# Kernel optimization log

Hardware: AMD Instinct MI355X
Metric: run time of the kernel (lower is better)

Reference implementation:

```python
import jax, jax.numpy as jnp
import numpy as np
from jax import lax

BN_EPS = 1e-5
DELTA_FRAC = 0.7


def ternarize(t):
    """Per-row (dim 0) ternarization: delta = 0.7*mean|t_i|, alpha = mean of |t_i| above delta."""
    B = t.shape[0]
    flat = t.reshape(B, -1)                       # [B, n]
    absf = jnp.abs(flat)
    n = flat.shape[1]
    d = DELTA_FRAC * absf.sum(axis=1) / n         # [B]
    mask = absf > d[:, None]                      # strict >, matching torch code
    count = mask.sum(axis=1).astype(flat.dtype)
    alpha = (absf * mask).sum(axis=1) / count     # [B]
    tern = jnp.where(flat > d[:, None], 1.0, 0.0) + jnp.where(flat < -d[:, None], -1.0, 0.0)
    return (tern * alpha[:, None]).reshape(t.shape)


def conv2d(x, w, b):
    out = lax.conv_general_dilated(x, w, window_strides=(1, 1), padding='VALID',
                                   dimension_numbers=('NCHW', 'OIHW', 'NCHW'))
    return out + b[None, :, None, None]


def maxpool2(x):
    return lax.reduce_window(x, -jnp.inf, lax.max, (1, 1, 2, 2), (1, 1, 2, 2), 'VALID')


def batchnorm_eval(x, gamma, beta):
    # eval-mode BN with running_mean=0, running_var=1
    inv = 1.0 / np.sqrt(1.0 + BN_EPS)
    return x * (gamma[None, :, None, None] * inv) + beta[None, :, None, None]


def setup_inputs() -> dict:
    key = jax.random.key(0)
    ks = jax.random.split(key, 12)
    B = 2048
    inp = {
        'x': jax.random.normal(ks[0], (B, 1, 28, 28), dtype=jnp.float32),
        'conv1_w': jax.random.normal(ks[1], (32, 1, 5, 5), dtype=jnp.float32) * 0.1,
        'conv1_b': jax.random.normal(ks[2], (32,), dtype=jnp.float32) * 0.1,
        'bn1_g': jax.random.normal(ks[3], (32,), dtype=jnp.float32) * 0.1 + 1.0,
        'bn1_b': jax.random.normal(ks[4], (32,), dtype=jnp.float32) * 0.1,
        'conv2_w': jax.random.normal(ks[5], (64, 32, 5, 5), dtype=jnp.float32) * 0.05,
        'conv2_b': jax.random.normal(ks[6], (64,), dtype=jnp.float32) * 0.1,
        'bn2_g': jax.random.normal(ks[7], (64,), dtype=jnp.float32) * 0.1 + 1.0,
        'bn2_b': jax.random.normal(ks[8], (64,), dtype=jnp.float32) * 0.1,
        'fc1_w': jax.random.normal(ks[9], (512, 1024), dtype=jnp.float32) * 0.03,
        'fc1_b': jax.random.normal(ks[10], (512,), dtype=jnp.float32) * 0.1,
        'fc2_w': jax.random.normal(ks[11], (10, 512), dtype=jnp.float32) * 0.05,
        'fc2_b': jnp.zeros((10,), dtype=jnp.float32),
    }
    return inp


def reference(x, conv1_w, conv1_b, bn1_g, bn1_b, conv2_w, conv2_b, bn2_g, bn2_b,
              fc1_w, fc1_b, fc2_w, fc2_b):
    h = ternarize(conv2d(x, conv1_w, conv1_b))            # [B,32,24,24]
    h = jax.nn.relu(maxpool2(batchnorm_eval(h, bn1_g, bn1_b)))  # [B,32,12,12]
    h = ternarize(conv2d(h, conv2_w, conv2_b))            # [B,64,8,8]
    h = jax.nn.relu(maxpool2(batchnorm_eval(h, bn2_g, bn2_b)))  # [B,64,4,4]
    h = h.reshape(-1, 1024)
    h = jax.nn.relu(ternarize(h @ fc1_w.T + fc1_b))       # [B,512]
    out = ternarize(h @ fc2_w.T + fc2_b)                  # [B,10]
    return out
```

## Files before the change

kernel.cpp:

```cpp
#include <hip/hip_runtime.h>

#define BATCH 2048

__device__ __forceinline__ float blockReduceSumF(float v, float* red, int tid, int nwaves) {
  #pragma unroll
  for (int off = 32; off > 0; off >>= 1) v += __shfl_xor(v, off);
  __syncthreads();
  if ((tid & 63) == 0) red[tid >> 6] = v;
  __syncthreads();
  if (tid == 0) {
    float s = red[0];
    for (int i = 1; i < nwaves; i++) s += red[i];
    red[31] = s;
  }
  __syncthreads();
  return red[31];
}

__device__ __forceinline__ float2 blockReduceSum2F(float a, float b, float* red, int tid, int nwaves) {
  #pragma unroll
  for (int off = 32; off > 0; off >>= 1) { a += __shfl_xor(a, off); b += __shfl_xor(b, off); }
  __syncthreads();
  if ((tid & 63) == 0) { red[tid >> 6] = a; red[(tid >> 6) + 16] = b; }
  __syncthreads();
  if (tid == 0) {
    float sa = red[0], sb = red[16];
    for (int i = 1; i < nwaves; i++) { sa += red[i]; sb += red[16 + i]; }
    red[30] = sa; red[31] = sb;
  }
  __syncthreads();
  return make_float2(red[30], red[31]);
}

__device__ __forceinline__ float groupReduce4w(float v, float* seg, int tj) {
  #pragma unroll
  for (int off = 32; off > 0; off >>= 1) v += __shfl_xor(v, off);
  __syncthreads();
  if ((tj & 63) == 0) seg[tj >> 6] = v;
  __syncthreads();
  return (seg[0] + seg[1]) + (seg[2] + seg[3]);
}

__global__ void k0_w2t(const float* __restrict__ w2, float* __restrict__ w2t) {
  int i = blockIdx.x * 256 + threadIdx.x;
  if (i >= 51200) return;
  int c2 = i / 800;
  int r = i - c2 * 800;
  w2t[r * 64 + c2] = w2[i];
}

__global__ __launch_bounds__(512, 6) void k1_conv1(
    const float* __restrict__ x, const float* __restrict__ w1, const float* __restrict__ b1,
    signed char* __restrict__ s1full, float* __restrict__ alpha1) {
  __shared__ float xs[784];
  __shared__ float wsm[800];
  __shared__ float red[32];

  const int tid = threadIdx.x;
  const int smp = blockIdx.x;

  for (int j = tid; j < 784; j += 512) xs[j] = x[smp * 784 + j];
  for (int j = tid; j < 800; j += 512) wsm[j] = w1[j];
  __syncthreads();

  const int c = tid >> 4;
  const int g = tid & 15;
  const float bias = b1[c];
  const float* wc = &wsm[c * 25];

  float a[36];
  float asum = 0.0f;
  #pragma unroll
  for (int tt = 0; tt < 3; tt++) {
    const int t = g + (tt << 4);
    const int r = t >> 1;
    const int hx = (t & 1) * 12;
    float acc[12];
    #pragma unroll
    for (int i = 0; i < 12; i++) acc[i] = bias;
    #pragma unroll
    for (int ky = 0; ky < 5; ky++) {
      const float* xp = &xs[(r + ky) * 28 + hx];
      float xrow[16];
      *(float4*)&xrow[0]  = *(const float4*)&xp[0];
      *(float4*)&xrow[4]  = *(const float4*)&xp[4];
      *(float4*)&xrow[8]  = *(const float4*)&xp[8];
      *(float4*)&xrow[12] = *(const float4*)&xp[12];
      #pragma unroll
      for (int kx = 0; kx < 5; kx++) {
        const float w = wc[ky * 5 + kx];
        #pragma unroll
        for (int i = 0; i < 12; i++) acc[i] = fmaf(xrow[i + kx], w, acc[i]);
      }
    }
    #pragma unroll
    for (int i = 0; i < 12; i++) { a[tt * 12 + i] = acc[i]; asum += fabsf(acc[i]); }
  }

  float tot = blockReduceSumF(asum, red, tid, 8);
  float delta = (0.7f * tot) / 18432.0f;

  float msum = 0.0f, mcnt = 0.0f;
  #pragma unroll
  for (int i = 0; i < 36; i++) {
    float fa = fabsf(a[i]);
    if (fa > delta) { msum += fa; mcnt += 1.0f; }
  }
  float2 mm = blockReduceSum2F(msum, mcnt, red, tid, 8);
  if (tid == 0) alpha1[smp] = (mm.y > 0.0f) ? (mm.x / mm.y) : 0.0f;

  signed char* sp = s1full + (size_t)smp * 18432 + c * 576 + g * 12;
  #pragma unroll
  for (int tt = 0; tt < 3; tt++) {
    #pragma unroll
    for (int i = 0; i < 12; i++) {
      float v = a[tt * 12 + i];
      int sv = (v > delta) ? 1 : ((v < -delta) ? -1 : 0);
      sp[tt * 192 + i] = (signed char)sv;
    }
  }
}

__global__ __launch_bounds__(256, 6) void k2_conv2(
    const signed char* __restrict__ s1full, const float* __restrict__ alpha1,
    const float* __restrict__ w2t, const float* __restrict__ b2,
    const float* __restrict__ g1, const float* __restrict__ bt1,
    signed char* __restrict__ s2full, float* __restrict__ alpha2) {
  __shared__ float pooled[4608];
  __shared__ float g1l[32], bt1l[32];
  __shared__ float red[32];

  const int tid = threadIdx.x;
  const int smp = blockIdx.x;
  const float BNINV = (float)(1.0 / sqrt(1.0 + 1e-5));

  if (tid < 32) { g1l[tid] = g1[tid] * BNINV; bt1l[tid] = bt1[tid]; }
  __syncthreads();

  const float a1 = alpha1[smp];
  for (int j = tid; j < 4608; j += 256) {
    int cc = j / 144;
    int r = j - cc * 144;
    int py = r / 12;
    int px = r - py * 12;
    const signed char* sp = s1full + (size_t)smp * 18432 + cc * 576 + (py * 2) * 24 + px * 2;
    float m = -1e30f;
    #pragma unroll
    for (int dy = 0; dy < 2; dy++)
      #pragma unroll
      for (int dx = 0; dx < 2; dx++) {
        float v = ((float)sp[dy * 24 + dx] * a1) * g1l[cc] + bt1l[cc];
        m = (v > m) ? v : m;
      }
    pooled[j] = (m > 0.0f) ? m : 0.0f;
  }
  __syncthreads();

  const int c2 = tid >> 2;
  const int q = tid & 3;
  const int r0 = q << 1;
  const float bias = b2[c2];
  float acc0[8], acc1[8];
  #pragma unroll
  for (int i = 0; i < 8; i++) { acc0[i] = bias; acc1[i] = bias; }

  for (int cc = 0; cc < 32; cc++) {
    const float* wt = w2t + cc * 1600 + c2;
    const float* pb = &pooled[cc * 144];
    float rows[2][12];
    *(float4*)&rows[0][0] = *(const float4*)&pb[r0 * 12];
    *(float4*)&rows[0][4] = *(const float4*)&pb[r0 * 12 + 4];
    *(float4*)&rows[0][8] = *(const float4*)&pb[r0 * 12 + 8];
    #pragma unroll
    for (int ky = 0; ky < 5; ky++) {
      float* B = rows[(ky + 1) & 1];
      const float* bp = &pb[(r0 + ky + 1) * 12];
      *(float4*)&B[0] = *(const float4*)&bp[0];
      *(float4*)&B[4] = *(const float4*)&bp[4];
      *(float4*)&B[8] = *(const float4*)&bp[8];
      const float* A = rows[ky & 1];
      #pragma unroll
      for (int kx = 0; kx < 5; kx++) {
        const float w = wt[(ky * 5 + kx) << 6];
        #pragma unroll
        for (int ox = 0; ox < 8; ox++) acc0[ox] = fmaf(A[ox + kx], w, acc0[ox]);
        #pragma unroll
        for (int ox = 0; ox < 8; ox++) acc1[ox] = fmaf(B[ox + kx], w, acc1[ox]);
      }
    }
  }

  float asum = 0.0f;
  #pragma unroll
  for (int i = 0; i < 8; i++) asum += fabsf(acc0[i]) + fabsf(acc1[i]);
  float tot = blockReduceSumF(asum, red, tid, 4);
  float delta = (0.7f * tot) / 4096.0f;

  float msum = 0.0f, mcnt = 0.0f;
  #pragma unroll
  for (int i = 0; i < 8; i++) {
    float f0 = fabsf(acc0[i]);
    if (f0 > delta) { msum += f0; mcnt += 1.0f; }
    float f1 = fabsf(acc1[i]);
    if (f1 > delta) { msum += f1; mcnt += 1.0f; }
  }
  float2 mm = blockReduceSum2F(msum, mcnt, red, tid, 4);
  if (tid == 0) alpha2[smp] = (mm.y > 0.0f) ? (mm.x / mm.y) : 0.0f;

  signed char* so = s2full + (size_t)smp * 4096 + c2 * 64 + r0 * 8;
  #pragma unroll
  for (int ox = 0; ox < 8; ox++) {
    float v = acc0[ox];
    so[ox] = (signed char)((v > delta) ? 1 : ((v < -delta) ? -1 : 0));
  }
  #pragma unroll
  for (int ox = 0; ox < 8; ox++) {
    float v = acc1[ox];
    so[8 + ox] = (signed char)((v > delta) ? 1 : ((v < -delta) ? -1 : 0));
  }
}

__global__ void k0_transpose(const float* __restrict__ w1f, float* __restrict__ w1t) {
  int i = blockIdx.x * 256 + threadIdx.x;
  int k = i >> 9;
  int o = i & 511;
  w1t[i] = w1f[o * 1024 + k];
}

__global__ __launch_bounds__(1024, 4) void k3_fc(
    const signed char* __restrict__ s2full, const float* __restrict__ alpha2,
    const float* __restrict__ w1t, const float* __restrict__ f1b,
    const float* __restrict__ w2f, const float* __restrict__ f2b,
    const float* __restrict__ g2, const float* __restrict__ bt2,
    float* __restrict__ out) {
  __shared__ float S[16384];
  __shared__ float fco[4][512];
  __shared__ float g2l[64], bt2l[64];
  __shared__ float redm[4][4];
  __shared__ float out2[4][10];

  const int tid = threadIdx.x;
  const int blk = blockIdx.x;
  const float BNINV = (float)(1.0 / sqrt(1.0 + 1e-5));

  if (tid < 64) { g2l[tid] = g2[tid] * BNINV; bt2l[tid] = bt2[tid]; }
  __syncthreads();

  float* h4 = S;
  for (int e = tid; e < 4096; e += 1024) {
    int j = e >> 2;
    int s = e & 3;
    int cc = j >> 4;
    int r = j & 15;
    int py = r >> 2;
    int px = r & 3;
    const signed char* sp = s2full + (size_t)(blk * 4 + s) * 4096 + cc * 64 + (py * 2) * 8 + px * 2;
    float a2 = alpha2[blk * 4 + s];
    float m = -1e30f;
    #pragma unroll
    for (int dy = 0; dy < 2; dy++)
      #pragma unroll
      for (int dx = 0; dx < 2; dx++) {
        float v = ((float)sp[dy * 8 + dx] * a2) * g2l[cc] + bt2l[cc];
        m = (v > m) ? v : m;
      }
    h4[j * 4 + s] = (m > 0.0f) ? m : 0.0f;
  }
  __syncthreads();

  const int kp = tid >> 7;
  const int og = tid & 127;
  float a00=0,a01=0,a02=0,a03=0, a10=0,a11=0,a12=0,a13=0;
  float a20=0,a21=0,a22=0,a23=0, a30=0,a31=0,a32=0,a33=0;
  const float4* w4 = (const float4*)w1t;
  const float4* h44 = (const float4*)h4;
  const int kbase = kp << 7;
  for (int kk = 0; kk < 128; kk++) {
    const int k = kbase + kk;
    const float4 wv = w4[(k << 7) + og];
    const float4 hv = h44[k];
    a00 = fmaf(hv.x, wv.x, a00); a01 = fmaf(hv.y, wv.x, a01);
    a02 = fmaf(hv.z, wv.x, a02); a03 = fmaf(hv.w, wv.x, a03);
    a10 = fmaf(hv.x, wv.y, a10); a11 = fmaf(hv.y, wv.y, a11);
    a12 = fmaf(hv.z, wv.y, a12); a13 = fmaf(hv.w, wv.y, a13);
    a20 = fmaf(hv.x, wv.z, a20); a21 = fmaf(hv.y, wv.z, a21);
    a22 = fmaf(hv.z, wv.z, a22); a23 = fmaf(hv.w, wv.z, a23);
    a30 = fmaf(hv.x, wv.w, a30); a31 = fmaf(hv.y, wv.w, a31);
    a32 = fmaf(hv.z, wv.w, a32); a33 = fmaf(hv.w, wv.w, a33);
  }
  __syncthreads();
  {
    float4* p4 = (float4*)S;
    const int base = (kp << 9) + (og << 2);
    p4[base + 0] = make_float4(a00, a01, a02, a03);
    p4[base + 1] = make_float4(a10, a11, a12, a13);
    p4[base + 2] = make_float4(a20, a21, a22, a23);
    p4[base + 3] = make_float4(a30, a31, a32, a33);
  }
  __syncthreads();

  for (int p = tid; p < 2048; p += 1024) {
    int o = p >> 2;
    int s = p & 3;
    float v = S[p];
    #pragma unroll
    for (int kp2 = 1; kp2 < 8; kp2++) v += S[kp2 * 2048 + p];
    fco[s][o] = v + f1b[o];
  }
  __syncthreads();

  float (*h3)[512] = (float(*)[512])S;
  const int sg = tid >> 8;
  const int tj = tid & 255;
  float v0 = fco[sg][tj];
  float v1 = fco[sg][tj + 256];
  float av0 = fabsf(v0), av1 = fabsf(v1);
  float tot = groupReduce4w(av0 + av1, redm[sg], tj);
  float delta = (0.7f * tot) / 512.0f;
  float m0 = (av0 > delta) ? av0 : 0.0f;
  float m1 = (av1 > delta) ? av1 : 0.0f;
  float msum = groupReduce4w(m0 + m1, redm[sg], tj);
  float mcnt = groupReduce4w(((av0 > delta) ? 1.0f : 0.0f) + ((av1 > delta) ? 1.0f : 0.0f),
                             redm[sg], tj);
  float alpha3 = (mcnt > 0.0f) ? (msum / mcnt) : 0.0f;
  {
    float t0 = (v0 > delta) ? 1.0f : ((v0 < -delta) ? -1.0f : 0.0f);
    float hv0 = t0 * alpha3;
    h3[sg][tj] = (hv0 > 0.0f) ? hv0 : 0.0f;
    float t1 = (v1 > delta) ? 1.0f : ((v1 < -delta) ? -1.0f : 0.0f);
    float hv1 = t1 * alpha3;
    h3[sg][tj + 256] = (hv1 > 0.0f) ? hv1 : 0.0f;
  }
  __syncthreads();

  const int lane = tid & 63;
  const int wid = tid >> 6;
  for (int t = wid; t < 40; t += 16) {
    int s = t / 10;
    int o = t - s * 10;
    float acc = 0.0f;
    #pragma unroll
    for (int m = 0; m < 8; m++) {
      int j = lane + (m << 6);
      acc = fmaf(h3[s][j], w2f[o * 512 + j], acc);
    }
    #pragma unroll
    for (int off = 32; off > 0; off >>= 1) acc += __shfl_xor(acc, off);
    if (lane == 0) out2[s][o] = acc + f2b[o];
  }
  __syncthreads();

  if (tid < 4) {
    int s = tid;
    float t2 = 0.0f;
    for (int i = 0; i < 10; i++) t2 += fabsf(out2[s][i]);
    float d = (0.7f * t2) / 10.0f;
    float ms = 0.0f, mc = 0.0f;
    for (int i = 0; i < 10; i++) {
      float a = fabsf(out2[s][i]);
      if (a > d) { ms += a; mc += 1.0f; }
    }
    float al = (mc > 0.0f) ? (ms / mc) : 0.0f;
    for (int i = 0; i < 10; i++) {
      float vv = out2[s][i];
      float sv = (vv > d) ? 1.0f : ((vv < -d) ? -1.0f : 0.0f);
      out[(size_t)(blk * 4 + s) * 10 + i] = sv * al;
    }
  }
}

__global__ void k_marker(float* __restrict__ out, int n, float val) {
  int i = blockIdx.x * 256 + threadIdx.x;
  if (i < n) out[i] = val;
}

extern "C" void kernel_launch(void* const* d_in, const int* in_sizes, int n_in,
                              void* d_out, int out_size, void* d_ws, size_t ws_size,
                              hipStream_t stream) {
  float* out = (float*)d_out;

  static const int expect[13] = {1605632, 800, 32, 32, 32, 51200, 64, 64, 64,
                                 524288, 512, 5120, 10};
  float marker = 0.0f;
  if (n_in != 13) marker = 304.0f;
  else {
    for (int i = 0; i < 13; i++)
      if (in_sizes[i] != expect[i]) { marker = 320.0f + 16.0f * i; break; }
  }
  if (marker == 0.0f && out_size != 20480) marker = 560.0f;

  float* alpha1 = (float*)d_ws;
  float* alpha2 = alpha1 + BATCH;
  float* w2t    = alpha2 + BATCH;
  signed char* s1full = (signed char*)(w2t + 51200);
  signed char* s2full = s1full + (size_t)BATCH * 18432;
  size_t needed = (size_t)((s2full + (size_t)BATCH * 4096) - (signed char*)d_ws);
  if (marker == 0.0f && ws_size < needed) marker = 576.0f;

  if (marker != 0.0f) {
    k_marker<<<dim3((out_size + 255) / 256), dim3(256), 0, stream>>>(out, out_size, marker);
    return;
  }

  const float* x   = (const float*)d_in[0];
  const float* c1w = (const float*)d_in[1];
  const float* c1b = (const float*)d_in[2];
  const float* g1  = (const float*)d_in[3];
  const float* bt1 = (const float*)d_in[4];
  const float* c2w = (const float*)d_in[5];
  const float* c2b = (const float*)d_in[6];
  const float* g2  = (const float*)d_in[7];
  const float* bt2 = (const float*)d_in[8];
  const float* f1w = (const float*)d_in[9];
  const float* f1b = (const float*)d_in[10];
  const float* f2w = (const float*)d_in[11];
  const float* f2b = (const float*)d_in[12];

  float* w1t = (float*)s1full;

  k0_w2t<<<dim3(200), dim3(256), 0, stream>>>(c2w, w2t);
  k1_conv1<<<dim3(BATCH), dim3(512), 0, stream>>>(x, c1w, c1b, s1full, alpha1);
  k2_conv2<<<dim3(BATCH), dim3(256), 0, stream>>>(s1full, alpha1, w2t, c2b, g1, bt1, s2full, alpha2);
  k0_transpose<<<dim3(2048), dim3(256), 0, stream>>>(f1w, w1t);
  k3_fc<<<dim3(BATCH / 4), dim3(1024), 0, stream>>>(s2full, alpha2, w1t, f1b, f2w, f2b, g2, bt2, out);
}
```

Baseline: 375.3 us.

## Process eight samples per FC block to halve fc1 weight traffic

```diff
diff --git a/kernel.cpp b/kernel.cpp
--- a/kernel.cpp
+++ b/kernel.cpp
@@ -32,13 +32,13 @@
   return make_float2(red[30], red[31]);
 }
 
-__device__ __forceinline__ float groupReduce4w(float v, float* seg, int tj) {
+__device__ __forceinline__ float groupReduce2w(float v, float* seg2, int tj) {
   #pragma unroll
   for (int off = 32; off > 0; off >>= 1) v += __shfl_xor(v, off);
   __syncthreads();
-  if ((tj & 63) == 0) seg[tj >> 6] = v;
-  __syncthreads();
-  return (seg[0] + seg[1]) + (seg[2] + seg[3]);
+  if ((tj & 63) == 0) seg2[tj >> 6] = v;
+  __syncthreads();
+  return seg2[0] + seg2[1];
 }
 
 __global__ void k0_w2t(const float* __restrict__ w2, float* __restrict__ w2t) {
@@ -227,35 +227,35 @@
   w1t[i] = w1f[o * 1024 + k];
 }
 
-__global__ __launch_bounds__(1024, 4) void k3_fc(
+__global__ __launch_bounds__(1024, 4) void k3_fc8(
     const signed char* __restrict__ s2full, const float* __restrict__ alpha2,
     const float* __restrict__ w1t, const float* __restrict__ f1b,
     const float* __restrict__ w2f, const float* __restrict__ f2b,
     const float* __restrict__ g2, const float* __restrict__ bt2,
     float* __restrict__ out) {
-  __shared__ float S[16384];
-  __shared__ float fco[4][512];
+  __shared__ float S[8192];
+  __shared__ float fco[8][512];
   __shared__ float g2l[64], bt2l[64];
-  __shared__ float redm[4][4];
-  __shared__ float out2[4][10];
+  __shared__ float seg[8][2];
+  __shared__ float out2[8][10];
 
   const int tid = threadIdx.x;
   const int blk = blockIdx.x;
   const float BNINV = (float)(1.0 / sqrt(1.0 + 1e-5));
 
   if (tid < 64) { g2l[tid] = g2[tid] * BNINV; bt2l[tid] = bt2[tid]; }
-  __syncthreads();
-
-  float* h4 = S;
-  for (int e = tid; e < 4096; e += 1024) {
-    int j = e >> 2;
-    int s = e & 3;
+  for (int p = tid; p < 4096; p += 1024) ((float*)fco)[p] = 0.0f;
+  __syncthreads();
+
+  for (int e = tid; e < 8192; e += 1024) {
+    int j = e >> 3;
+    int s = e & 7;
     int cc = j >> 4;
     int r = j & 15;
     int py = r >> 2;
     int px = r & 3;
-    const signed char* sp = s2full + (size_t)(blk * 4 + s) * 4096 + cc * 64 + (py * 2) * 8 + px * 2;
-    float a2 = alpha2[blk * 4 + s];
+    const signed char* sp = s2full + (size_t)(blk * 8 + s) * 4096 + cc * 64 + (py * 2) * 8 + px * 2;
+    float a2 = alpha2[blk * 8 + s];
     float m = -1e30f;
     #pragma unroll
     for (int dy = 0; dy < 2; dy++)
@@ -264,78 +264,83 @@
         float v = ((float)sp[dy * 8 + dx] * a2) * g2l[cc] + bt2l[cc];
         m = (v > m) ? v : m;
       }
-    h4[j * 4 + s] = (m > 0.0f) ? m : 0.0f;
+    S[j * 8 + s] = (m > 0.0f) ? m : 0.0f;
   }
   __syncthreads();
 
   const int kp = tid >> 7;
   const int og = tid & 127;
-  float a00=0,a01=0,a02=0,a03=0, a10=0,a11=0,a12=0,a13=0;
-  float a20=0,a21=0,a22=0,a23=0, a30=0,a31=0,a32=0,a33=0;
-  const float4* w4 = (const float4*)w1t;
-  const float4* h44 = (const float4*)h4;
-  const int kbase = kp << 7;
-  for (int kk = 0; kk < 128; kk++) {
-    const int k = kbase + kk;
-    const float4 wv = w4[(k << 7) + og];
-    const float4 hv = h44[k];
-    a00 = fmaf(hv.x, wv.x, a00); a01 = fmaf(hv.y, wv.x, a01);
-    a02 = fmaf(hv.z, wv.x, a02); a03 = fmaf(hv.w, wv.x, a03);
-    a10 = fmaf(hv.x, wv.y, a10); a11 = fmaf(hv.y, wv.y, a11);
-    a12 = fmaf(hv.z, wv.y, a12); a13 = fmaf(hv.w, wv.y, a13);
-    a20 = fmaf(hv.x, wv.z, a20); a21 = fmaf(hv.y, wv.z, a21);
-    a22 = fmaf(hv.z, wv.z, a22); a23 = fmaf(hv.w, wv.z, a23);
-    a30 = fmaf(hv.x, wv.w, a30); a31 = fmaf(hv.y, wv.w, a31);
-    a32 = fmaf(hv.z, wv.w, a32); a33 = fmaf(hv.w, wv.w, a33);
-  }
-  __syncthreads();
+  float ac[8][4];
+  #pragma unroll
+  for (int s = 0; s < 8; s++)
+    #pragma unroll
+    for (int i = 0; i < 4; i++) ac[s][i] = 0.0f;
+
   {
-    float4* p4 = (float4*)S;
-    const int base = (kp << 9) + (og << 2);
-    p4[base + 0] = make_float4(a00, a01, a02, a03);
-    p4[base + 1] = make_float4(a10, a11, a12, a13);
-    p4[base + 2] = make_float4(a20, a21, a22, a23);
-    p4[base + 3] = make_float4(a30, a31, a32, a33);
-  }
-  __syncthreads();
-
-  for (int p = tid; p < 2048; p += 1024) {
-    int o = p >> 2;
-    int s = p & 3;
-    float v = S[p];
-    #pragma unroll
-    for (int kp2 = 1; kp2 < 8; kp2++) v += S[kp2 * 2048 + p];
-    fco[s][o] = v + f1b[o];
+    const float4* w4 = (const float4*)w1t;
+    const float4* h84 = (const float4*)S;
+    const int kbase = kp << 7;
+    for (int kk = 0; kk < 128; kk++) {
+      const int k = kbase + kk;
+      const float4 wv = w4[(k << 7) + og];
+      const float4 h0 = h84[2 * k];
+      const float4 h1 = h84[2 * k + 1];
+      float hs[8] = {h0.x, h0.y, h0.z, h0.w, h1.x, h1.y, h1.z, h1.w};
+      #pragma unroll
+      for (int s = 0; s < 8; s++) {
+        ac[s][0] = fmaf(hs[s], wv.x, ac[s][0]);
+        ac[s][1] = fmaf(hs[s], wv.y, ac[s][1]);
+        ac[s][2] = fmaf(hs[s], wv.z, ac[s][2]);
+        ac[s][3] = fmaf(hs[s], wv.w, ac[s][3]);
+      }
+    }
+  }
+
+  #pragma unroll 1
+  for (int j = 0; j < 8; j++) {
+    if (kp == j) {
+      #pragma unroll
+      for (int s = 0; s < 8; s++)
+        #pragma unroll
+        for (int i = 0; i < 4; i++)
+          fco[s][og * 4 + i] += ac[s][i];
+    }
+    __syncthreads();
+  }
+  for (int p = tid; p < 4096; p += 1024) {
+    int s = p >> 9;
+    int o = p & 511;
+    fco[s][o] += f1b[o];
   }
   __syncthreads();
 
   float (*h3)[512] = (float(*)[512])S;
-  const int sg = tid >> 8;
-  const int tj = tid & 255;
-  float v0 = fco[sg][tj];
-  float v1 = fco[sg][tj + 256];
-  float av0 = fabsf(v0), av1 = fabsf(v1);
-  float tot = groupReduce4w(av0 + av1, redm[sg], tj);
+  const int sg = tid >> 7;
+  const int tj = tid & 127;
+  float v[4], av[4];
+  #pragma unroll
+  for (int i = 0; i < 4; i++) { v[i] = fco[sg][tj + (i << 7)]; av[i] = fabsf(v[i]); }
+  float tot = groupReduce2w(((av[0] + av[1]) + (av[2] + av[3])), seg[sg], tj);
   float delta = (0.7f * tot) / 512.0f;
-  float m0 = (av0 > delta) ? av0 : 0.0f;
-  float m1 = (av1 > delta) ? av1 : 0.0f;
-  float msum = groupReduce4w(m0 + m1, redm[sg], tj);
-  float mcnt = groupReduce4w(((av0 > delta) ? 1.0f : 0.0f) + ((av1 > delta) ? 1.0f : 0.0f),
-                             redm[sg], tj);
+  float msum = 0.0f, mcnt = 0.0f;
+  #pragma unroll
+  for (int i = 0; i < 4; i++) {
+    if (av[i] > delta) { msum += av[i]; mcnt += 1.0f; }
+  }
+  msum = groupReduce2w(msum, seg[sg], tj);
+  mcnt = groupReduce2w(mcnt, seg[sg], tj);
   float alpha3 = (mcnt > 0.0f) ? (msum / mcnt) : 0.0f;
-  {
-    float t0 = (v0 > delta) ? 1.0f : ((v0 < -delta) ? -1.0f : 0.0f);
-    float hv0 = t0 * alpha3;
-    h3[sg][tj] = (hv0 > 0.0f) ? hv0 : 0.0f;
-    float t1 = (v1 > delta) ? 1.0f : ((v1 < -delta) ? -1.0f : 0.0f);
-    float hv1 = t1 * alpha3;
-    h3[sg][tj + 256] = (hv1 > 0.0f) ? hv1 : 0.0f;
+  #pragma unroll
+  for (int i = 0; i < 4; i++) {
+    float t = (v[i] > delta) ? 1.0f : ((v[i] < -delta) ? -1.0f : 0.0f);
+    float hv = t * alpha3;
+    h3[sg][tj + (i << 7)] = (hv > 0.0f) ? hv : 0.0f;
   }
   __syncthreads();
 
   const int lane = tid & 63;
   const int wid = tid >> 6;
-  for (int t = wid; t < 40; t += 16) {
+  for (int t = wid; t < 80; t += 16) {
     int s = t / 10;
     int o = t - s * 10;
     float acc = 0.0f;
@@ -350,7 +355,7 @@
   }
   __syncthreads();
 
-  if (tid < 4) {
+  if (tid < 8) {
     int s = tid;
     float t2 = 0.0f;
     for (int i = 0; i < 10; i++) t2 += fabsf(out2[s][i]);
@@ -364,7 +369,7 @@
     for (int i = 0; i < 10; i++) {
       float vv = out2[s][i];
       float sv = (vv > d) ? 1.0f : ((vv < -d) ? -1.0f : 0.0f);
-      out[(size_t)(blk * 4 + s) * 10 + i] = sv * al;
+      out[(size_t)(blk * 8 + s) * 10 + i] = sv * al;
     }
   }
 }
@@ -422,5 +427,5 @@
   k1_conv1<<<dim3(BATCH), dim3(512), 0, stream>>>(x, c1w, c1b, s1full, alpha1);
   k2_conv2<<<dim3(BATCH), dim3(256), 0, stream>>>(s1full, alpha1, w2t, c2b, g1, bt1, s2full, alpha2);
   k0_transpose<<<dim3(2048), dim3(256), 0, stream>>>(f1w, w1t);
-  k3_fc<<<dim3(BATCH / 4), dim3(1024), 0, stream>>>(s2full, alpha2, w1t, f1b, f2w, f2b, g2, bt2, out);
-}
+  k3_fc8<<<dim3(BATCH / 8), dim3(1024), 0, stream>>>(s2full, alpha2, w1t, f1b, f2w, f2b, g2, bt2, out);
+}
```

Result: no change. 380.6 us (+1.4%).
